# Performance work log

Measured on AMD Instinct MI355X. Metric: run time of the kernel, lower is better.

The kernel has to match this reference:

```python
import jax, jax.numpy as jnp
import numpy as np

C = 512
H = 8  # num_heads
GROUPS = 32
EPS = 1e-5


def group_norm(x, scale, bias):
    # x: [b, c, h, w]; GroupNorm(32, c) normalizes over (c//32, h, w) per group
    b, c, h, w = x.shape
    xg = x.reshape(b, GROUPS, c // GROUPS * h * w)
    mean = jnp.mean(xg, axis=-1, keepdims=True)
    var = jnp.var(xg, axis=-1, keepdims=True)
    xg = (xg - mean) * jax.lax.rsqrt(var + EPS)
    x = xg.reshape(b, c, h, w)
    return x * scale[None, :, None, None] + bias[None, :, None, None]


def setup_inputs() -> dict:
    key = jax.random.key(0)
    ks = jax.random.split(key, 6)
    init = 0.02
    return {
        "x": jax.random.normal(ks[0], (8, C, 32, 32), dtype=jnp.float32),
        "gn_scale": jnp.ones((C,), jnp.float32),
        "gn_bias": jnp.zeros((C,), jnp.float32),
        "Wq": jax.random.normal(ks[1], (C, C), jnp.float32) * init,
        "bq": jnp.zeros((C,), jnp.float32),
        "Wk": jax.random.normal(ks[2], (C, C), jnp.float32) * init,
        "bk": jnp.zeros((C,), jnp.float32),
        "Wv": jax.random.normal(ks[3], (C, C), jnp.float32) * init,
        "bv": jnp.zeros((C,), jnp.float32),
        "Wo": jax.random.normal(ks[4], (C, C), jnp.float32) * init,
        "bo": jnp.zeros((C,), jnp.float32),
    }


def reference(x, gn_scale, gn_bias, Wq, bq, Wk, bk, Wv, bv, Wo, bo):
    b, c, h, w = x.shape
    s = h * w  # number of spatial tokens
    d = c // H  # head dim
    residual = x
    xn = group_norm(x, gn_scale, gn_bias)
    t = xn.reshape(b, c, s).transpose(0, 2, 1)  # [b, s, c]
    # torch Linear: y = x @ W.T + b
    q = t @ Wq.T + bq
    k = t @ Wk.T + bk
    v = t @ Wv.T + bv
    q = q.reshape(b, s, H, d).transpose(0, 2, 1, 3)  # [b, H, s, d]
    k = k.reshape(b, s, H, d).transpose(0, 2, 1, 3)
    v = v.reshape(b, s, H, d).transpose(0, 2, 1, 3)
    scale = d ** -0.5
    attn = jnp.einsum('bhqd,bhkd->bhqk', q, k) * scale  # [b, H, s, s]
    attn = jax.nn.softmax(attn, axis=-1)
    out = jnp.einsum('bhqk,bhkd->bhqd', attn, v)  # [b, H, s, d]
    out = out.transpose(0, 2, 1, 3).reshape(b, s, c)
    out = out @ Wo.T + bo
    out = out.transpose(0, 2, 1).reshape(b, c, h, w)
    return out + residual
```

## Files before the change

kernel.cpp:

```cpp
#include <hip/hip_runtime.h>


typedef __bf16 bf16x8 __attribute__((ext_vector_type(8)));
typedef __bf16 bf16x4 __attribute__((ext_vector_type(4)));
typedef float floatx4 __attribute__((ext_vector_type(4)));

static __device__ __forceinline__ floatx4 mfma16(bf16x8 a, bf16x8 b, floatx4 c) {
  return __builtin_amdgcn_mfma_f32_16x16x32_bf16(a, b, c, 0, 0, 0);
}

static __device__ __forceinline__ void async_cp16(const void* g, void* l) {
  __builtin_amdgcn_global_load_lds(
      (const __attribute__((address_space(1))) unsigned int*)g,
      (__attribute__((address_space(3))) unsigned int*)l, 16, 0, 0);
}

__global__ __launch_bounds__(256) void prep_gn_kernel(
    const float* __restrict__ x, const float* __restrict__ gamma,
    const float* __restrict__ beta,
    const float* __restrict__ Wq, const float* __restrict__ bq,
    const float* __restrict__ Wk, const float* __restrict__ bk,
    const float* __restrict__ Wv, const float* __restrict__ bv,
    const float* __restrict__ Wo,
    __bf16* __restrict__ wqkv, __bf16* __restrict__ wo,
    float* __restrict__ bqkv, __bf16* __restrict__ t) {
  __shared__ __bf16 tile[16 * 1024];
  __shared__ float rbuf[8];
  int tid = threadIdx.x;
  int bx = blockIdx.x;

  if (bx >= 256) {
    const float SC = 0.125f * 1.4426950408889634f;
    int i = ((bx - 256) * 256 + tid) * 4;
    float4 q4 = *(const float4*)(Wq + i);
    float4 k4 = *(const float4*)(Wk + i);
    float4 v4 = *(const float4*)(Wv + i);
    float4 o4 = *(const float4*)(Wo + i);
    *(bf16x4*)(wqkv + i) = (bf16x4){(__bf16)(q4.x * SC), (__bf16)(q4.y * SC),
                                    (__bf16)(q4.z * SC), (__bf16)(q4.w * SC)};
    *(bf16x4*)(wqkv + 262144 + i) =
        (bf16x4){(__bf16)k4.x, (__bf16)k4.y, (__bf16)k4.z, (__bf16)k4.w};
    *(bf16x4*)(wqkv + 524288 + i) =
        (bf16x4){(__bf16)v4.x, (__bf16)v4.y, (__bf16)v4.z, (__bf16)v4.w};
    *(bf16x4*)(wo + i) =
        (bf16x4){(__bf16)o4.x, (__bf16)o4.y, (__bf16)o4.z, (__bf16)o4.w};
    int j = (bx - 256) * 256 + tid;
    if (j < 512) {
      bqkv[j]        = bq[j] * SC;
      bqkv[512 + j]  = bk[j];
      bqkv[1024 + j] = bv[j];
    }
    return;
  }

  int b = bx >> 5, g = bx & 31;
  const float* xp = x + (size_t)(b * 512 + g * 16) * 1024;
  const float4* xp4 = (const float4*)xp;

  float sacc = 0.f, ssacc = 0.f;
#pragma unroll
  for (int it = 0; it < 16; ++it) {
    float4 v = xp4[it * 256 + tid];
    sacc += v.x + v.y + v.z + v.w;
    ssacc += v.x * v.x + v.y * v.y + v.z * v.z + v.w * v.w;
  }
#pragma unroll
  for (int off = 1; off < 64; off <<= 1) {
    sacc += __shfl_xor(sacc, off);
    ssacc += __shfl_xor(ssacc, off);
  }
  int wv = tid >> 6;
  if ((tid & 63) == 0) { rbuf[wv] = sacc; rbuf[4 + wv] = ssacc; }
  __syncthreads();
  float S1 = rbuf[0] + rbuf[1] + rbuf[2] + rbuf[3];
  float S2 = rbuf[4] + rbuf[5] + rbuf[6] + rbuf[7];
  float mean = S1 * (1.f / 16384.f);
  float var = S2 * (1.f / 16384.f) - mean * mean;
  float inv = rsqrtf(var + 1e-5f);

#pragma unroll
  for (int it = 0; it < 16; ++it) {
    float4 v = xp4[it * 256 + tid];
    float ga = gamma[g * 16 + it], be = beta[g * 16 + it];
    int base = it * 1024 + tid * 4;
    tile[base + 0] = (__bf16)((v.x - mean) * inv * ga + be);
    tile[base + 1] = (__bf16)((v.y - mean) * inv * ga + be);
    tile[base + 2] = (__bf16)((v.z - mean) * inv * ga + be);
    tile[base + 3] = (__bf16)((v.w - mean) * inv * ga + be);
  }
  __syncthreads();

#pragma unroll
  for (int j = 0; j < 8; ++j) {
    int qid = j * 256 + tid;
    int sidx = qid >> 1, half = qid & 1;
    union { uint4 u; __bf16 h[8]; } o;
#pragma unroll
    for (int i = 0; i < 8; ++i) o.h[i] = tile[(half * 8 + i) * 1024 + sidx];
    *(uint4*)(t + (size_t)(b * 1024 + sidx) * 512 + g * 16 + half * 8) = o.u;
  }
}

__global__ __launch_bounds__(256) void gemm_qkv_kernel(
    const __bf16* __restrict__ t, const __bf16* __restrict__ wqkv,
    const float* __restrict__ bqkv,
    __bf16* __restrict__ qb, __bf16* __restrict__ kb, __bf16* __restrict__ vt) {
  __shared__ __align__(16) __bf16 smem[8192];
  __bf16* As = smem;
  __bf16* Bs = smem + 4096;
  int tid = threadIdx.x;
  int m0 = blockIdx.x * 128;
  int n0 = blockIdx.y * 128;
  int wave = tid >> 6, lane = tid & 63;
  int l15 = lane & 15, quad = lane >> 4;
  int wm = wave >> 1, wn = wave & 1;

  floatx4 acc[4][4];
#pragma unroll
  for (int mi = 0; mi < 4; ++mi)
#pragma unroll
    for (int ni = 0; ni < 4; ++ni) acc[mi][ni] = (floatx4){0.f, 0.f, 0.f, 0.f};

  int r1 = tid >> 2, o1 = (tid & 3) * 8;
  const __bf16* gA1 = t + (size_t)(m0 + r1) * 512 + o1;
  const __bf16* gA2 = t + (size_t)(m0 + 64 + r1) * 512 + o1;
  const __bf16* gB1 = wqkv + (size_t)(n0 + r1) * 512 + o1;
  const __bf16* gB2 = wqkv + (size_t)(n0 + 64 + r1) * 512 + o1;
  __bf16* lA1 = As + tid * 8;
  __bf16* lA2 = As + 2048 + tid * 8;
  __bf16* lB1 = Bs + tid * 8;
  __bf16* lB2 = Bs + 2048 + tid * 8;

  for (int k0 = 0; k0 < 512; k0 += 32) {
    async_cp16(gA1 + k0, lA1);
    async_cp16(gA2 + k0, lA2);
    async_cp16(gB1 + k0, lB1);
    async_cp16(gB2 + k0, lB2);
    __syncthreads();
    bf16x8 af[4], bfr[4];
#pragma unroll
    for (int mi = 0; mi < 4; ++mi)
      af[mi] = *(const bf16x8*)&As[(wm * 64 + mi * 16 + l15) * 32 + quad * 8];
#pragma unroll
    for (int ni = 0; ni < 4; ++ni)
      bfr[ni] = *(const bf16x8*)&Bs[(wn * 64 + ni * 16 + l15) * 32 + quad * 8];
#pragma unroll
    for (int mi = 0; mi < 4; ++mi)
#pragma unroll
      for (int ni = 0; ni < 4; ++ni)
        acc[mi][ni] = mfma16(af[mi], bfr[ni], acc[mi][ni]);
    __syncthreads();
  }

  int mat = n0 >> 9;
  int bidx = m0 >> 10, s0 = m0 & 1023;
  int hA = (n0 & 511) >> 6;
  float bias[4];
#pragma unroll
  for (int ni = 0; ni < 4; ++ni)
    bias[ni] = bqkv[n0 + wn * 64 + ni * 16 + l15];

  if (mat < 2) {
    __bf16* dst = (mat == 0) ? qb : kb;
    for (int c = 0; c < 4; ++c) {
      if ((c >> 1) == wm) {
#pragma unroll
        for (int mi2 = 0; mi2 < 2; ++mi2) {
          int mi = (c & 1) * 2 + mi2;
          int lrow = mi2 * 16 + quad * 4;
#pragma unroll
          for (int ni = 0; ni < 4; ++ni)
#pragma unroll
            for (int r = 0; r < 4; ++r)
              smem[(lrow + r) * 136 + wn * 64 + ni * 16 + l15] =
                  (__bf16)(acc[mi][ni][r] + bias[ni]);
        }
      }
      __syncthreads();
#pragma unroll
      for (int u = 0; u < 2; ++u) {
        int f = tid * 16 + u * 8;
        int row = f >> 7, col = f & 127;
        uint4 val = *(uint4*)&smem[row * 136 + col];
        int head = hA + (col >> 6), d = col & 63;
        *(uint4*)(dst + ((size_t)(bidx * 8 + head) * 1024 + s0 + c * 32 + row) * 64 + d) = val;
      }
      __syncthreads();
    }
  } else {
    for (int c = 0; c < 4; ++c) {
      if ((c >> 1) == wn) {
#pragma unroll
        for (int ni2 = 0; ni2 < 2; ++ni2) {
          int ni = (c & 1) * 2 + ni2;
          int nrow = ni2 * 16 + l15;
#pragma unroll
          for (int mi = 0; mi < 4; ++mi)
#pragma unroll
            for (int r = 0; r < 4; ++r)
              smem[nrow * 136 + wm * 64 + mi * 16 + quad * 4 + r] =
                  (__bf16)(acc[mi][ni][r] + bias[ni]);
        }
      }
      __syncthreads();
#pragma unroll
      for (int u = 0; u < 2; ++u) {
        int f = tid * 16 + u * 8;
        int nrow = f >> 7, mcol = f & 127;
        uint4 val = *(uint4*)&smem[nrow * 136 + mcol];
        int nloc = c * 32 + nrow;
        int head = hA + (nloc >> 6), d = nloc & 63;
        *(uint4*)(vt + ((size_t)(bidx * 8 + head) * 64 + d) * 1024 + s0 + mcol) = val;
      }
      __syncthreads();
    }
  }
}

__global__ __launch_bounds__(256) void attn_kernel(
    const __bf16* __restrict__ qb, const __bf16* __restrict__ kb,
    const __bf16* __restrict__ vt, __bf16* __restrict__ ao) {
  __shared__ __align__(16) __bf16 Ks[2][64 * 72];
  __shared__ __align__(16) __bf16 Vs[2][64 * 72];
  __shared__ __align__(16) __bf16 Ps[128 * 72];
  int tid = threadIdx.x;
  int bx = blockIdx.x;
  int b = bx >> 6, h = (bx >> 3) & 7, q128 = bx & 7;
  int wv = tid >> 6, lane = tid & 63, l15 = lane & 15, quad = lane >> 4;
  size_t bh = (size_t)(b * 8 + h) * 65536;
  const __bf16* Qp = qb + bh;
  const __bf16* Kp = kb + bh;
  const __bf16* Vp = vt + bh;
  int q0 = q128 * 128, qw = q0 + wv * 32;

  bf16x8 aq[2][2];
#pragma unroll
  for (int mi = 0; mi < 2; ++mi)
#pragma unroll
    for (int kh = 0; kh < 2; ++kh)
      aq[mi][kh] = *(const bf16x8*)(Qp + (size_t)(qw + mi * 16 + l15) * 64 + kh * 32 + quad * 8);

  bf16x8 ones;
#pragma unroll
  for (int i = 0; i < 8; ++i) ones[i] = (__bf16)1.0f;

  floatx4 oacc[2][4], lacc[2];
#pragma unroll
  for (int mi = 0; mi < 2; ++mi) {
    lacc[mi] = (floatx4){0.f, 0.f, 0.f, 0.f};
#pragma unroll
    for (int di = 0; di < 4; ++di) oacc[mi][di] = (floatx4){0.f, 0.f, 0.f, 0.f};
  }

  int srow = tid >> 3, scol = (tid & 7) * 8;
  int ldsoff = srow * 72 + scol;

  uint4 kr0, kr1, vr0, vr1;
  kr0 = *(const uint4*)(Kp + (size_t)srow * 64 + scol);
  kr1 = *(const uint4*)(Kp + (size_t)(srow + 32) * 64 + scol);
  vr0 = *(const uint4*)(Vp + (size_t)srow * 1024 + scol);
  vr1 = *(const uint4*)(Vp + (size_t)(srow + 32) * 1024 + scol);

  for (int kt = 0; kt < 16; ++kt) {
    int cur = kt & 1;
    *(uint4*)&Ks[cur][ldsoff] = kr0;
    *(uint4*)&Ks[cur][ldsoff + 32 * 72] = kr1;
    *(uint4*)&Vs[cur][ldsoff] = vr0;
    *(uint4*)&Vs[cur][ldsoff + 32 * 72] = vr1;
    if (kt < 15) {
      int nt = kt + 1;
      kr0 = *(const uint4*)(Kp + (size_t)(nt * 64 + srow) * 64 + scol);
      kr1 = *(const uint4*)(Kp + (size_t)(nt * 64 + srow + 32) * 64 + scol);
      vr0 = *(const uint4*)(Vp + (size_t)srow * 1024 + nt * 64 + scol);
      vr1 = *(const uint4*)(Vp + (size_t)(srow + 32) * 1024 + nt * 64 + scol);
    }
    __syncthreads();

    floatx4 sa[2][4];
#pragma unroll
    for (int ni = 0; ni < 4; ++ni) {
      bf16x8 bk0 = *(const bf16x8*)&Ks[cur][(ni * 16 + l15) * 72 + quad * 8];
      bf16x8 bk1 = *(const bf16x8*)&Ks[cur][(ni * 16 + l15) * 72 + 32 + quad * 8];
#pragma unroll
      for (int mi = 0; mi < 2; ++mi) {
        floatx4 s4 = (floatx4){0.f, 0.f, 0.f, 0.f};
        s4 = mfma16(bk0, aq[mi][0], s4);
        s4 = mfma16(bk1, aq[mi][1], s4);
        sa[mi][ni] = s4;
      }
    }

#pragma unroll
    for (int mi = 0; mi < 2; ++mi)
#pragma unroll
      for (int ni = 0; ni < 4; ++ni) {
        bf16x4 pk;
#pragma unroll
        for (int r = 0; r < 4; ++r)
          pk[r] = (__bf16)__builtin_amdgcn_exp2f(sa[mi][ni][r]);
        *(bf16x4*)&Ps[(wv * 32 + mi * 16 + l15) * 72 + ni * 16 + quad * 4] = pk;
      }

    bf16x8 ap[2][2];
#pragma unroll
    for (int mi = 0; mi < 2; ++mi) {
      ap[mi][0] = *(const bf16x8*)&Ps[(wv * 32 + mi * 16 + l15) * 72 + quad * 8];
      ap[mi][1] = *(const bf16x8*)&Ps[(wv * 32 + mi * 16 + l15) * 72 + 32 + quad * 8];
    }
#pragma unroll
    for (int di = 0; di < 4; ++di) {
      bf16x8 bv0 = *(const bf16x8*)&Vs[cur][(di * 16 + l15) * 72 + quad * 8];
      bf16x8 bv1 = *(const bf16x8*)&Vs[cur][(di * 16 + l15) * 72 + 32 + quad * 8];
#pragma unroll
      for (int mi = 0; mi < 2; ++mi) {
        oacc[mi][di] = mfma16(ap[mi][0], bv0, oacc[mi][di]);
        oacc[mi][di] = mfma16(ap[mi][1], bv1, oacc[mi][di]);
      }
    }
#pragma unroll
    for (int mi = 0; mi < 2; ++mi) {
      lacc[mi] = mfma16(ap[mi][0], ones, lacc[mi]);
      lacc[mi] = mfma16(ap[mi][1], ones, lacc[mi]);
    }
  }

#pragma unroll
  for (int mi = 0; mi < 2; ++mi)
#pragma unroll
    for (int r = 0; r < 4; ++r) {
      float invl = 1.f / lacc[mi][r];
      int lrow = wv * 32 + mi * 16 + quad * 4 + r;
#pragma unroll
      for (int di = 0; di < 4; ++di)
        Ps[lrow * 72 + di * 16 + l15] = (__bf16)(oacc[mi][di][r] * invl);
    }
  __syncthreads();
  __bf16* aop = ao + (size_t)b * 524288 + h * 64;
#pragma unroll
  for (int u = 0; u < 4; ++u) {
    int idx = u * 256 + tid;
    int row = idx >> 3, col = (idx & 7) * 8;
    *(uint4*)(aop + (size_t)(q0 + row) * 512 + col) = *(uint4*)&Ps[row * 72 + col];
  }
}

__global__ __launch_bounds__(256) void gemm_out_kernel(
    const __bf16* __restrict__ ao, const __bf16* __restrict__ wo,
    const float* __restrict__ bo, const float* __restrict__ x,
    float* __restrict__ out) {
  __shared__ __align__(16) __bf16 As[128 * 32];
  __shared__ __align__(16) __bf16 Bs[64 * 32];
  __shared__ __align__(16) float ctile[32 * 132];
  int tid = threadIdx.x;
  int m0 = blockIdx.x * 128;
  int n0 = blockIdx.y * 64;
  int wave = tid >> 6, lane = tid & 63;
  int l15 = lane & 15, quad = lane >> 4;
  int wm = wave >> 1, wn = wave & 1;

  floatx4 acc[4][2];
#pragma unroll
  for (int mi = 0; mi < 4; ++mi)
#pragma unroll
    for (int ni = 0; ni < 2; ++ni) acc[mi][ni] = (floatx4){0.f, 0.f, 0.f, 0.f};

  int r1 = tid >> 2, o1 = (tid & 3) * 8;
  const __bf16* gA1 = ao + (size_t)(m0 + r1) * 512 + o1;
  const __bf16* gA2 = ao + (size_t)(m0 + 64 + r1) * 512 + o1;
  const __bf16* gB1 = wo + (size_t)(n0 + r1) * 512 + o1;
  __bf16* lA1 = As + tid * 8;
  __bf16* lA2 = As + 2048 + tid * 8;
  __bf16* lB1 = Bs + tid * 8;

  for (int k0 = 0; k0 < 512; k0 += 32) {
    async_cp16(gA1 + k0, lA1);
    async_cp16(gA2 + k0, lA2);
    async_cp16(gB1 + k0, lB1);
    __syncthreads();
    bf16x8 af[4], bfr[2];
#pragma unroll
    for (int mi = 0; mi < 4; ++mi)
      af[mi] = *(const bf16x8*)&As[(wm * 64 + mi * 16 + l15) * 32 + quad * 8];
#pragma unroll
    for (int ni = 0; ni < 2; ++ni)
      bfr[ni] = *(const bf16x8*)&Bs[(wn * 32 + ni * 16 + l15) * 32 + quad * 8];
#pragma unroll
    for (int mi = 0; mi < 4; ++mi)
#pragma unroll
      for (int ni = 0; ni < 2; ++ni)
        acc[mi][ni] = mfma16(af[mi], bfr[ni], acc[mi][ni]);
    __syncthreads();
  }

  int b = m0 >> 10, s0 = m0 & 1023;
  for (int cc = 0; cc < 2; ++cc) {
    __syncthreads();
    if (wn == cc) {
#pragma unroll
      for (int ni = 0; ni < 2; ++ni) {
        int nn = ni * 16 + l15;
        float bias = bo[n0 + cc * 32 + nn];
#pragma unroll
        for (int mi = 0; mi < 4; ++mi)
#pragma unroll
          for (int r = 0; r < 4; ++r)
            ctile[nn * 132 + wm * 64 + mi * 16 + quad * 4 + r] =
                acc[mi][ni][r] + bias;
      }
    }
    __syncthreads();
    int nn = tid >> 3, mlb = (tid & 7) * 16;
    int n = n0 + cc * 32 + nn;
    const float* xr = x + (size_t)(b * 512 + n) * 1024 + s0;
    float* orow = out + (size_t)(b * 512 + n) * 1024 + s0;
#pragma unroll
    for (int i = 0; i < 16; i += 4) {
      float4 cv = *(float4*)&ctile[nn * 132 + mlb + i];
      float4 xv = *(const float4*)&xr[mlb + i];
      float4 ov = {cv.x + xv.x, cv.y + xv.y, cv.z + xv.z, cv.w + xv.w};
      *(float4*)&orow[mlb + i] = ov;
    }
  }
}

extern "C" void kernel_launch(void* const* d_in, const int* in_sizes, int n_in,
                              void* d_out, int out_size, void* d_ws, size_t ws_size,
                              hipStream_t stream) {
  const float* x  = (const float*)d_in[0];
  const float* gs = (const float*)d_in[1];
  const float* gb = (const float*)d_in[2];
  const float* Wq = (const float*)d_in[3];
  const float* bq = (const float*)d_in[4];
  const float* Wk = (const float*)d_in[5];
  const float* bk = (const float*)d_in[6];
  const float* Wv = (const float*)d_in[7];
  const float* bv = (const float*)d_in[8];
  const float* Wo = (const float*)d_in[9];
  const float* bo = (const float*)d_in[10];
  float* out = (float*)d_out;

  char* ws = (char*)d_ws;
  __bf16* wqkv = (__bf16*)(ws);
  __bf16* wo   = (__bf16*)(ws + 1572864);
  float*  bqkv = (float*)(ws + 2097152);
  __bf16* t    = (__bf16*)(ws + 2103296);
  __bf16* ao   = t;
  __bf16* qb   = (__bf16*)(ws + 10491904);
  __bf16* kb   = (__bf16*)(ws + 18880512);
  __bf16* vtb  = (__bf16*)(ws + 27269120);

  prep_gn_kernel<<<dim3(512), dim3(256), 0, stream>>>(
      x, gs, gb, Wq, bq, Wk, bk, Wv, bv, Wo, wqkv, wo, bqkv, t);
  gemm_qkv_kernel<<<dim3(64, 12), dim3(256), 0, stream>>>(t, wqkv, bqkv, qb, kb, vtb);
  attn_kernel<<<dim3(512), dim3(256), 0, stream>>>(qb, kb, vtb, ao);
  gemm_out_kernel<<<dim3(64, 8), dim3(256), 0, stream>>>(ao, wo, bo, x, out);
}
```

Measured before the change: 157.6 us.

## Store Q/K/V and attention probabilities in FP8 and use FP8 MFMA

The QKV GEMM epilogue now converts Q, K and V^T to FP8 before storing them. The attention kernel then runs QK^T, PV and the row-sum through fp8 16x16x32 MFMA, with probabilities also packed to FP8 in LDS. This halves global and LDS traffic for Q/K/V and halves K/V staging loads. The cost is much lower numerical precision, which risks exceeding accuracy tolerances.

```diff
diff --git a/kernel.cpp b/kernel.cpp
--- a/kernel.cpp
+++ b/kernel.cpp
@@ -7,12 +7,27 @@
 
 static __device__ __forceinline__ floatx4 mfma16(bf16x8 a, bf16x8 b, floatx4 c) {
   return __builtin_amdgcn_mfma_f32_16x16x32_bf16(a, b, c, 0, 0, 0);
+}
+static __device__ __forceinline__ floatx4 mfma_fp8(long a, long b, floatx4 c) {
+  return __builtin_amdgcn_mfma_f32_16x16x32_fp8_fp8(a, b, c, 0, 0, 0);
 }
 
 static __device__ __forceinline__ void async_cp16(const void* g, void* l) {
   __builtin_amdgcn_global_load_lds(
       (const __attribute__((address_space(1))) unsigned int*)g,
       (__attribute__((address_space(3))) unsigned int*)l, 16, 0, 0);
+}
+
+static __device__ __forceinline__ uint2 cvt8_bf16_fp8(uint4 v) {
+  union { uint4 u; __bf16 h[8]; } in; in.u = v;
+  float f[8];
+#pragma unroll
+  for (int i = 0; i < 8; ++i) f[i] = (float)in.h[i];
+  int lo = __builtin_amdgcn_cvt_pk_fp8_f32(f[0], f[1], 0, false);
+  lo = __builtin_amdgcn_cvt_pk_fp8_f32(f[2], f[3], lo, true);
+  int hi = __builtin_amdgcn_cvt_pk_fp8_f32(f[4], f[5], 0, false);
+  hi = __builtin_amdgcn_cvt_pk_fp8_f32(f[6], f[7], hi, true);
+  return uint2{(unsigned)lo, (unsigned)hi};
 }
 
 __global__ __launch_bounds__(256) void prep_gn_kernel(
@@ -104,7 +119,8 @@
 __global__ __launch_bounds__(256) void gemm_qkv_kernel(
     const __bf16* __restrict__ t, const __bf16* __restrict__ wqkv,
     const float* __restrict__ bqkv,
-    __bf16* __restrict__ qb, __bf16* __restrict__ kb, __bf16* __restrict__ vt) {
+    unsigned char* __restrict__ qb, unsigned char* __restrict__ kb,
+    unsigned char* __restrict__ vt) {
   __shared__ __align__(16) __bf16 smem[8192];
   __bf16* As = smem;
   __bf16* Bs = smem + 4096;
@@ -161,7 +177,7 @@
     bias[ni] = bqkv[n0 + wn * 64 + ni * 16 + l15];
 
   if (mat < 2) {
-    __bf16* dst = (mat == 0) ? qb : kb;
+    unsigned char* dst = (mat == 0) ? qb : kb;
     for (int c = 0; c < 4; ++c) {
       if ((c >> 1) == wm) {
 #pragma unroll
@@ -181,9 +197,9 @@
       for (int u = 0; u < 2; ++u) {
         int f = tid * 16 + u * 8;
         int row = f >> 7, col = f & 127;
-        uint4 val = *(uint4*)&smem[row * 136 + col];
+        uint2 val = cvt8_bf16_fp8(*(uint4*)&smem[row * 136 + col]);
         int head = hA + (col >> 6), d = col & 63;
-        *(uint4*)(dst + ((size_t)(bidx * 8 + head) * 1024 + s0 + c * 32 + row) * 64 + d) = val;
+        *(uint2*)(dst + ((size_t)(bidx * 8 + head) * 1024 + s0 + c * 32 + row) * 64 + d) = val;
       }
       __syncthreads();
     }
@@ -207,10 +223,10 @@
       for (int u = 0; u < 2; ++u) {
         int f = tid * 16 + u * 8;
         int nrow = f >> 7, mcol = f & 127;
-        uint4 val = *(uint4*)&smem[nrow * 136 + mcol];
+        uint2 val = cvt8_bf16_fp8(*(uint4*)&smem[nrow * 136 + mcol]);
         int nloc = c * 32 + nrow;
         int head = hA + (nloc >> 6), d = nloc & 63;
-        *(uint4*)(vt + ((size_t)(bidx * 8 + head) * 64 + d) * 1024 + s0 + mcol) = val;
+        *(uint2*)(vt + ((size_t)(bidx * 8 + head) * 64 + d) * 1024 + s0 + mcol) = val;
       }
       __syncthreads();
     }
@@ -218,31 +234,30 @@
 }
 
 __global__ __launch_bounds__(256) void attn_kernel(
-    const __bf16* __restrict__ qb, const __bf16* __restrict__ kb,
-    const __bf16* __restrict__ vt, __bf16* __restrict__ ao) {
-  __shared__ __align__(16) __bf16 Ks[2][64 * 72];
-  __shared__ __align__(16) __bf16 Vs[2][64 * 72];
+    const unsigned char* __restrict__ qb, const unsigned char* __restrict__ kb,
+    const unsigned char* __restrict__ vt, __bf16* __restrict__ ao) {
+  __shared__ __align__(16) unsigned char Ks[2][64 * 80];
+  __shared__ __align__(16) unsigned char Vs[2][64 * 80];
   __shared__ __align__(16) __bf16 Ps[128 * 72];
+  unsigned char* Psb = (unsigned char*)Ps;
   int tid = threadIdx.x;
   int bx = blockIdx.x;
   int b = bx >> 6, h = (bx >> 3) & 7, q128 = bx & 7;
   int wv = tid >> 6, lane = tid & 63, l15 = lane & 15, quad = lane >> 4;
   size_t bh = (size_t)(b * 8 + h) * 65536;
-  const __bf16* Qp = qb + bh;
-  const __bf16* Kp = kb + bh;
-  const __bf16* Vp = vt + bh;
+  const unsigned char* Qp = qb + bh;
+  const unsigned char* Kp = kb + bh;
+  const unsigned char* Vp = vt + bh;
   int q0 = q128 * 128, qw = q0 + wv * 32;
 
-  bf16x8 aq[2][2];
+  long aq[2][2];
 #pragma unroll
   for (int mi = 0; mi < 2; ++mi)
 #pragma unroll
     for (int kh = 0; kh < 2; ++kh)
-      aq[mi][kh] = *(const bf16x8*)(Qp + (size_t)(qw + mi * 16 + l15) * 64 + kh * 32 + quad * 8);
-
-  bf16x8 ones;
-#pragma unroll
-  for (int i = 0; i < 8; ++i) ones[i] = (__bf16)1.0f;
+      aq[mi][kh] = *(const long*)(Qp + (size_t)(qw + mi * 16 + l15) * 64 + kh * 32 + quad * 8);
+
+  const long ONES = 0x3838383838383838L;
 
   floatx4 oacc[2][4], lacc[2];
 #pragma unroll
@@ -252,40 +267,34 @@
     for (int di = 0; di < 4; ++di) oacc[mi][di] = (floatx4){0.f, 0.f, 0.f, 0.f};
   }
 
-  int srow = tid >> 3, scol = (tid & 7) * 8;
-  int ldsoff = srow * 72 + scol;
-
-  uint4 kr0, kr1, vr0, vr1;
-  kr0 = *(const uint4*)(Kp + (size_t)srow * 64 + scol);
-  kr1 = *(const uint4*)(Kp + (size_t)(srow + 32) * 64 + scol);
-  vr0 = *(const uint4*)(Vp + (size_t)srow * 1024 + scol);
-  vr1 = *(const uint4*)(Vp + (size_t)(srow + 32) * 1024 + scol);
+  int srow = tid >> 2, scol = (tid & 3) * 16;
+  int ldsoff = srow * 80 + scol;
+
+  uint4 kr, vr;
+  kr = *(const uint4*)(Kp + (size_t)srow * 64 + scol);
+  vr = *(const uint4*)(Vp + (size_t)srow * 1024 + scol);
 
   for (int kt = 0; kt < 16; ++kt) {
     int cur = kt & 1;
-    *(uint4*)&Ks[cur][ldsoff] = kr0;
-    *(uint4*)&Ks[cur][ldsoff + 32 * 72] = kr1;
-    *(uint4*)&Vs[cur][ldsoff] = vr0;
-    *(uint4*)&Vs[cur][ldsoff + 32 * 72] = vr1;
+    *(uint4*)&Ks[cur][ldsoff] = kr;
+    *(uint4*)&Vs[cur][ldsoff] = vr;
     if (kt < 15) {
       int nt = kt + 1;
-      kr0 = *(const uint4*)(Kp + (size_t)(nt * 64 + srow) * 64 + scol);
-      kr1 = *(const uint4*)(Kp + (size_t)(nt * 64 + srow + 32) * 64 + scol);
-      vr0 = *(const uint4*)(Vp + (size_t)srow * 1024 + nt * 64 + scol);
-      vr1 = *(const uint4*)(Vp + (size_t)(srow + 32) * 1024 + nt * 64 + scol);
+      kr = *(const uint4*)(Kp + (size_t)(nt * 64 + srow) * 64 + scol);
+      vr = *(const uint4*)(Vp + (size_t)srow * 1024 + nt * 64 + scol);
     }
     __syncthreads();
 
     floatx4 sa[2][4];
 #pragma unroll
     for (int ni = 0; ni < 4; ++ni) {
-      bf16x8 bk0 = *(const bf16x8*)&Ks[cur][(ni * 16 + l15) * 72 + quad * 8];
-      bf16x8 bk1 = *(const bf16x8*)&Ks[cur][(ni * 16 + l15) * 72 + 32 + quad * 8];
+      long bk0 = *(const long*)&Ks[cur][(ni * 16 + l15) * 80 + quad * 8];
+      long bk1 = *(const long*)&Ks[cur][(ni * 16 + l15) * 80 + 32 + quad * 8];
 #pragma unroll
       for (int mi = 0; mi < 2; ++mi) {
         floatx4 s4 = (floatx4){0.f, 0.f, 0.f, 0.f};
-        s4 = mfma16(bk0, aq[mi][0], s4);
-        s4 = mfma16(bk1, aq[mi][1], s4);
+        s4 = mfma_fp8(bk0, aq[mi][0], s4);
+        s4 = mfma_fp8(bk1, aq[mi][1], s4);
         sa[mi][ni] = s4;
       }
     }
@@ -294,36 +303,40 @@
     for (int mi = 0; mi < 2; ++mi)
 #pragma unroll
       for (int ni = 0; ni < 4; ++ni) {
-        bf16x4 pk;
-#pragma unroll
-        for (int r = 0; r < 4; ++r)
-          pk[r] = (__bf16)__builtin_amdgcn_exp2f(sa[mi][ni][r]);
-        *(bf16x4*)&Ps[(wv * 32 + mi * 16 + l15) * 72 + ni * 16 + quad * 4] = pk;
-      }
-
-    bf16x8 ap[2][2];
+        float e0 = __builtin_amdgcn_exp2f(sa[mi][ni][0]);
+        float e1 = __builtin_amdgcn_exp2f(sa[mi][ni][1]);
+        float e2 = __builtin_amdgcn_exp2f(sa[mi][ni][2]);
+        float e3 = __builtin_amdgcn_exp2f(sa[mi][ni][3]);
+        int pk = __builtin_amdgcn_cvt_pk_fp8_f32(e0, e1, 0, false);
+        pk = __builtin_amdgcn_cvt_pk_fp8_f32(e2, e3, pk, true);
+        *(unsigned int*)&Psb[(wv * 32 + mi * 16 + l15) * 72 + ni * 16 + quad * 4] =
+            (unsigned)pk;
+      }
+
+    long ap[2][2];
 #pragma unroll
     for (int mi = 0; mi < 2; ++mi) {
-      ap[mi][0] = *(const bf16x8*)&Ps[(wv * 32 + mi * 16 + l15) * 72 + quad * 8];
-      ap[mi][1] = *(const bf16x8*)&Ps[(wv * 32 + mi * 16 + l15) * 72 + 32 + quad * 8];
+      ap[mi][0] = *(const long*)&Psb[(wv * 32 + mi * 16 + l15) * 72 + quad * 8];
+      ap[mi][1] = *(const long*)&Psb[(wv * 32 + mi * 16 + l15) * 72 + 32 + quad * 8];
     }
 #pragma unroll
     for (int di = 0; di < 4; ++di) {
-      bf16x8 bv0 = *(const bf16x8*)&Vs[cur][(di * 16 + l15) * 72 + quad * 8];
-      bf16x8 bv1 = *(const bf16x8*)&Vs[cur][(di * 16 + l15) * 72 + 32 + quad * 8];
+      long bv0 = *(const long*)&Vs[cur][(di * 16 + l15) * 80 + quad * 8];
+      long bv1 = *(const long*)&Vs[cur][(di * 16 + l15) * 80 + 32 + quad * 8];
 #pragma unroll
       for (int mi = 0; mi < 2; ++mi) {
-        oacc[mi][di] = mfma16(ap[mi][0], bv0, oacc[mi][di]);
-        oacc[mi][di] = mfma16(ap[mi][1], bv1, oacc[mi][di]);
+        oacc[mi][di] = mfma_fp8(ap[mi][0], bv0, oacc[mi][di]);
+        oacc[mi][di] = mfma_fp8(ap[mi][1], bv1, oacc[mi][di]);
       }
     }
 #pragma unroll
     for (int mi = 0; mi < 2; ++mi) {
-      lacc[mi] = mfma16(ap[mi][0], ones, lacc[mi]);
-      lacc[mi] = mfma16(ap[mi][1], ones, lacc[mi]);
-    }
-  }
-
+      lacc[mi] = mfma_fp8(ap[mi][0], ONES, lacc[mi]);
+      lacc[mi] = mfma_fp8(ap[mi][1], ONES, lacc[mi]);
+    }
+  }
+
+  __syncthreads();
 #pragma unroll
   for (int mi = 0; mi < 2; ++mi)
 #pragma unroll
@@ -445,9 +458,9 @@
   float*  bqkv = (float*)(ws + 2097152);
   __bf16* t    = (__bf16*)(ws + 2103296);
   __bf16* ao   = t;
-  __bf16* qb   = (__bf16*)(ws + 10491904);
-  __bf16* kb   = (__bf16*)(ws + 18880512);
-  __bf16* vtb  = (__bf16*)(ws + 27269120);
+  unsigned char* qb = (unsigned char*)(ws + 10491904);
+  unsigned char* kb = (unsigned char*)(ws + 14686208);
+  unsigned char* vtb = (unsigned char*)(ws + 18880512);
 
   prep_gn_kernel<<<dim3(512), dim3(256), 0, stream>>>(
       x, gs, gb, Wq, bq, Wk, bk, Wv, bv, Wo, wqkv, wo, bqkv, t);
```

Measured after the change: 148.6 us. 5.7% less time.
